# Kernel optimization log

Measured on AMD Instinct MI355X. Metric: run time of the kernel, lower is better.

Reference implementation:

```python
import jax, jax.numpy as jnp
import numpy as np

B, T, C, H = 128, 256, 384, 6
D = C // H  # head dim = 64


def setup_inputs() -> dict:
    key = jax.random.key(0)
    k1, k2, k3, k4, k5 = jax.random.split(key, 5)
    s = 0.02
    return {
        "x": jax.random.normal(k1, (B, T, C), dtype=jnp.float32),
        "W_qkv": jax.random.normal(k2, (C, 3 * C), dtype=jnp.float32) * s,
        "b_qkv": jax.random.normal(k3, (3 * C,), dtype=jnp.float32) * s,
        "W_proj": jax.random.normal(k4, (C, C), dtype=jnp.float32) * s,
        "b_proj": jax.random.normal(k5, (C,), dtype=jnp.float32) * s,
    }


def reference(x, W_qkv, b_qkv, W_proj, b_proj):
    Bv, Tv, Cv = x.shape
    # fused QKV projection, then split
    qkv = x @ W_qkv + b_qkv                      # [B,T,3C]
    q, k, v = jnp.split(qkv, 3, axis=-1)
    # [B,T,C] -> [B,H,T,D]
    q = q.reshape(Bv, Tv, H, D).transpose(0, 2, 1, 3)
    k = k.reshape(Bv, Tv, H, D).transpose(0, 2, 1, 3)
    v = v.reshape(Bv, Tv, H, D).transpose(0, 2, 1, 3)
    # causal masked scores, scaled by head_dim**-0.5
    scores = jnp.einsum("bhqd,bhkd->bhqk", q, k) * (D ** -0.5)
    causal = jnp.tril(jnp.ones((Tv, Tv), dtype=bool))
    scores = jnp.where(causal, scores, -jnp.inf)
    wt = jax.nn.softmax(scores, axis=-1)
    # dropout layers are identity in eval mode
    out = jnp.einsum("bhqk,bhkd->bhqd", wt, v)   # [B,H,T,D]
    out = out.transpose(0, 2, 1, 3).reshape(Bv, Tv, Cv)
    return out @ W_proj + b_proj
```

## Files before the change

### kernel.cpp

```cpp
#include <hip/hip_runtime.h>

typedef unsigned short u16;
typedef unsigned int u32;
typedef __attribute__((ext_vector_type(4))) float f32x4;
typedef __attribute__((ext_vector_type(8))) __bf16 bf16x8;
typedef __attribute__((ext_vector_type(2))) __bf16 bf16x2;

#define NEGINF (-1e30f)
#define QSCALE 0.18033688011112042f

__device__ __forceinline__ u16 f32_to_bf16(float f) {
  union { float f; unsigned int u; } v;
  v.f = f;
  unsigned int u = v.u;
  u += 0x7fffu + ((u >> 16) & 1u);
  return (u16)(u >> 16);
}

__device__ __forceinline__ u32 pk_bf16(float a, float b) {
  bf16x2 t;
  t.x = (__bf16)a;
  t.y = (__bf16)b;
  return __builtin_bit_cast(u32, t);
}

__device__ __forceinline__ f32x4 mfma_bf16(bf16x8 a, bf16x8 b, f32x4 c) {
  return __builtin_amdgcn_mfma_f32_16x16x32_bf16(a, b, c, 0, 0, 0);
}

#define GLOAD_LDS16(g, l) __builtin_amdgcn_global_load_lds( \
    (const __attribute__((address_space(1))) unsigned int*)(g), \
    (__attribute__((address_space(3))) unsigned int*)(l), 16, 0, 0)

__global__ void k_cvt_all(const float4* __restrict__ x4, u16* __restrict__ xb,
                          const float* __restrict__ Wqkv, u16* __restrict__ wqkvb,
                          const float* __restrict__ Wproj, u16* __restrict__ wprojb) {
  const int bidx = (int)blockIdx.x;
  if (bidx < 12288) {
    int i = bidx * 256 + threadIdx.x;
    float4 v = x4[i];
    uint2 o;
    o.x = (unsigned int)f32_to_bf16(v.x) | ((unsigned int)f32_to_bf16(v.y) << 16);
    o.y = (unsigned int)f32_to_bf16(v.z) | ((unsigned int)f32_to_bf16(v.w) << 16);
    *(uint2*)(xb + (size_t)i * 4) = o;
  } else if (bidx < 14016) {
    int idx = (bidx - 12288) * 256 + threadIdx.x;
    if (idx < 384 * 1152) {
      int k = idx / 1152, n = idx - k * 1152;
      wqkvb[(size_t)n * 384 + k] = f32_to_bf16(Wqkv[idx]);
    }
  } else {
    int idx = (bidx - 14016) * 256 + threadIdx.x;
    if (idx < 384 * 384) {
      int k = idx / 384, n = idx - k * 384;
      wprojb[(size_t)n * 384 + k] = f32_to_bf16(Wproj[idx]);
    }
  }
}

template <bool SW>
__device__ __forceinline__ void gemm256x64(
    const u16* __restrict__ A, const u16* __restrict__ Bt,
    int mBase, int nBase, u16* lsA, u16* lsB,
    f32x4 acc[4][2], int lane, int wv, int wm, int wn) {
  const int l15 = lane & 15;
  size_t aoff[4];
  u32 aldso[4];
#pragma unroll
  for (int jj = 0; jj < 4; ++jj) {
    int c = wv * 256 + jj * 64 + lane;
    int row = c >> 3;
    int kc = (c & 7) ^ (row & 7);
    aoff[jj] = (size_t)(mBase + row) * 384 + kc * 8;
    aldso[jj] = (u32)(wv * 256 + jj * 64) * 8;
  }
  int cb = wv * 64 + lane;
  int brow = cb >> 3;
  size_t boff = (size_t)(nBase + brow) * 384 + (size_t)(((cb & 7) ^ (brow & 7)) * 8);
  u32 bldso = (u32)(wv * 64) * 8;

#define STAGE_T(kt, buf) do { \
  _Pragma("unroll") \
  for (int jj = 0; jj < 4; ++jj) \
    GLOAD_LDS16(A + aoff[jj] + (kt), lsA + (buf) * 16384 + aldso[jj]); \
  GLOAD_LDS16(Bt + boff + (kt), lsB + (buf) * 4096 + bldso); \
  } while (0)

  STAGE_T(0, 0);
#pragma unroll
  for (int t = 0; t < 6; ++t) {
    const int cur = t & 1;
    if (t < 5) {
      STAGE_T((t + 1) * 64, cur ^ 1);
      asm volatile("s_waitcnt vmcnt(5)" ::: "memory");
    } else {
      asm volatile("s_waitcnt vmcnt(0)" ::: "memory");
    }
    __builtin_amdgcn_s_barrier();
    const char* bA = (const char*)(lsA + cur * 16384);
    const char* bB = (const char*)(lsB + cur * 4096);
#pragma unroll
    for (int ks = 0; ks < 2; ++ks) {
      bf16x8 af[4], bfr[2];
#pragma unroll
      for (int i = 0; i < 4; ++i) {
        int row = wm * 64 + i * 16 + l15;
        af[i] = *(const bf16x8*)(bA + row * 128 + (((ks * 4 + (lane >> 4)) ^ (row & 7)) << 4));
      }
#pragma unroll
      for (int j = 0; j < 2; ++j) {
        int row = wn * 32 + j * 16 + l15;
        bfr[j] = *(const bf16x8*)(bB + row * 128 + (((ks * 4 + (lane >> 4)) ^ (row & 7)) << 4));
      }
#pragma unroll
      for (int i = 0; i < 4; ++i)
#pragma unroll
        for (int j = 0; j < 2; ++j)
          acc[i][j] = SW ? mfma_bf16(bfr[j], af[i], acc[i][j])
                         : mfma_bf16(af[i], bfr[j], acc[i][j]);
    }
    __builtin_amdgcn_s_barrier();
  }
#undef STAGE_T
}

__global__ __launch_bounds__(512, 4) void k_qkv(
    const u16* __restrict__ A, const u16* __restrict__ Bt,
    const float* __restrict__ bias,
    u16* __restrict__ Qb, u16* __restrict__ Kb, u16* __restrict__ Vtb) {
  __shared__ __align__(16) u16 lsA[2 * 16384];
  __shared__ __align__(16) u16 lsB[2 * 4096];
  const int tid = threadIdx.x, lane = tid & 63, wv = tid >> 6;
  const int l15 = lane & 15, g = lane >> 4;
  const int wm = wv >> 1, wn = wv & 1;
  const int bid = (int)blockIdx.x;
  const int wgid = (bid & 7) * 288 + (bid >> 3);
  const int mtile = wgid / 18, ntile = wgid % 18;
  const int mBase = mtile * 256, nBase = ntile * 64;
  const int part = ntile / 6;
  const int hh = ntile % 6;
  char* ot = (char*)lsA;

  f32x4 acc[4][2] = {};
  if (part == 2) {
    gemm256x64<false>(A, Bt, mBase, nBase, lsA, lsB, acc, lane, wv, wm, wn);
#pragma unroll
    for (int j = 0; j < 2; ++j) {
      int drow = wn * 32 + j * 16 + l15;
      float bv = bias[nBase + drow];
#pragma unroll
      for (int i = 0; i < 4; ++i) {
        int t0 = wm * 64 + i * 16 + g * 4;
        uint2 w;
        w.x = pk_bf16(acc[i][j][0] + bv, acc[i][j][1] + bv);
        w.y = pk_bf16(acc[i][j][2] + bv, acc[i][j][3] + bv);
        int byte = (drow * 512 + t0 * 2) ^ ((drow & 7) << 4);
        *(uint2*)(ot + byte) = w;
      }
    }
    asm volatile("s_waitcnt lgkmcnt(0)" ::: "memory");
    __builtin_amdgcn_s_barrier();
    size_t obase = (size_t)(mtile * 6 + hh) * (64 * 256);
#pragma unroll
    for (int p = 0; p < 4; ++p) {
      int idx = p * 512 + tid;
      int row = idx >> 5, c = idx & 31;
      uint4 v = *(const uint4*)(ot + row * 512 + (((c ^ (row & 7)) << 4)));
      *(uint4*)(Vtb + obase + (size_t)row * 256 + c * 8) = v;
    }
  } else {
    gemm256x64<true>(A, Bt, mBase, nBase, lsA, lsB, acc, lane, wv, wm, wn);
    const float scale = (part == 0) ? QSCALE : 1.0f;
    u16* dst = (part == 0) ? Qb : Kb;
#pragma unroll
    for (int j = 0; j < 2; ++j) {
      int dbase = wn * 32 + j * 16 + g * 4;
      float4 bv4 = *(const float4*)(bias + nBase + dbase);
#pragma unroll
      for (int i = 0; i < 4; ++i) {
        int trow = wm * 64 + i * 16 + l15;
        uint2 w;
        w.x = pk_bf16((acc[i][j][0] + bv4.x) * scale, (acc[i][j][1] + bv4.y) * scale);
        w.y = pk_bf16((acc[i][j][2] + bv4.z) * scale, (acc[i][j][3] + bv4.w) * scale);
        int byte = (trow * 128 + dbase * 2) ^ ((trow & 7) << 4);
        *(uint2*)(ot + byte) = w;
      }
    }
    asm volatile("s_waitcnt lgkmcnt(0)" ::: "memory");
    __builtin_amdgcn_s_barrier();
    size_t obase = (size_t)(mtile * 6 + hh) * (256 * 64);
#pragma unroll
    for (int p = 0; p < 4; ++p) {
      int idx = p * 512 + tid;
      int row = idx >> 3, c = idx & 7;
      uint4 v = *(const uint4*)(ot + row * 128 + (((c ^ (row & 7)) << 4)));
      *(uint4*)(dst + obase + (size_t)row * 64 + c * 8) = v;
    }
  }
}

__global__ __launch_bounds__(256, 3) void k_attn(
    const u16* __restrict__ Qb, const u16* __restrict__ Kb,
    const u16* __restrict__ Vtb, u16* __restrict__ Ob) {
  __shared__ __align__(16) u16 lsP[4][32 * 64];
  const int lane = threadIdx.x & 63, wv = threadIdx.x >> 6;
  const int l15 = lane & 15, g = lane >> 4;
  const int s = blockIdx.y ? (5 - wv) : ((wv < 2) ? 7 - wv : 3 - wv);
  const int bh = blockIdx.x;
  const int b = bh / 6, h = bh % 6;
  const u16* Qh = Qb + (size_t)bh * (256 * 64);
  const u16* Kh = Kb + (size_t)bh * (256 * 64);
  const u16* Vh = Vtb + (size_t)bh * (64 * 256);
  const int ktiles = (s >> 1) + 1;
  char* pbuf = (char*)&lsP[wv][0];

  bf16x8 qf[2][2];
#pragma unroll
  for (int ks = 0; ks < 2; ++ks)
#pragma unroll
    for (int iq = 0; iq < 2; ++iq)
      qf[ks][iq] = *(const bf16x8*)(Qh + (size_t)(s * 32 + iq * 16 + l15) * 64 + ks * 32 + g * 8);

  f32x4 o[4][2] = {};
  float rl[2] = {0.f, 0.f};

#pragma unroll 1
  for (int kt = 0; kt < ktiles; ++kt) {
    bf16x8 kf[2][4];
#pragma unroll
    for (int ks = 0; ks < 2; ++ks)
#pragma unroll
      for (int jk = 0; jk < 4; ++jk)
        kf[ks][jk] = *(const bf16x8*)(Kh + (size_t)(kt * 64 + jk * 16 + l15) * 64 + ks * 32 + g * 8);

    f32x4 st[4][2] = {};
    __builtin_amdgcn_s_setprio(1);
#pragma unroll
    for (int ks = 0; ks < 2; ++ks)
#pragma unroll
      for (int jk = 0; jk < 4; ++jk)
#pragma unroll
        for (int iq = 0; iq < 2; ++iq)
          st[jk][iq] = mfma_bf16(kf[ks][jk], qf[ks][iq], st[jk][iq]);
    __builtin_amdgcn_s_setprio(0);

    bf16x8 vf[2][4];
#pragma unroll
    for (int ks = 0; ks < 2; ++ks)
#pragma unroll
      for (int jd = 0; jd < 4; ++jd)
        vf[ks][jd] = *(const bf16x8*)(Vh + (size_t)(jd * 16 + l15) * 256 + kt * 64 + ks * 32 + g * 8);

    if (kt == ktiles - 1) {
#pragma unroll
      for (int jk = 0; jk < 4; ++jk)
#pragma unroll
        for (int iq = 0; iq < 2; ++iq)
#pragma unroll
          for (int r = 0; r < 4; ++r)
            if (kt * 64 + jk * 16 + g * 4 + r > s * 32 + iq * 16 + l15)
              st[jk][iq][r] = NEGINF;
    }

    float rs[2] = {0.f, 0.f};
#pragma unroll
    for (int jk = 0; jk < 4; ++jk)
#pragma unroll
      for (int iq = 0; iq < 2; ++iq) {
        float p0 = __builtin_amdgcn_exp2f(st[jk][iq][0]);
        float p1 = __builtin_amdgcn_exp2f(st[jk][iq][1]);
        float p2 = __builtin_amdgcn_exp2f(st[jk][iq][2]);
        float p3 = __builtin_amdgcn_exp2f(st[jk][iq][3]);
        rs[iq] += (p0 + p1) + (p2 + p3);
        int q = iq * 16 + l15;
        int byte = (q * 128 + (jk * 16 + g * 4) * 2) ^ ((q & 7) << 4);
        uint2 w;
        w.x = pk_bf16(p0, p1);
        w.y = pk_bf16(p2, p3);
        *(uint2*)(pbuf + byte) = w;
      }
#pragma unroll
    for (int iq = 0; iq < 2; ++iq) {
      float v = rs[iq];
      v += __shfl_xor(v, 16);
      v += __shfl_xor(v, 32);
      rl[iq] += v;
    }

#pragma unroll
    for (int ks = 0; ks < 2; ++ks) {
      bf16x8 pf[2];
#pragma unroll
      for (int iq = 0; iq < 2; ++iq) {
        int q = iq * 16 + l15;
        pf[iq] = *(const bf16x8*)(pbuf + ((q * 128 + ks * 64 + g * 16) ^ ((q & 7) << 4)));
      }
      __builtin_amdgcn_s_setprio(1);
#pragma unroll
      for (int jd = 0; jd < 4; ++jd)
#pragma unroll
        for (int iq = 0; iq < 2; ++iq)
          o[jd][iq] = mfma_bf16(vf[ks][jd], pf[iq], o[jd][iq]);
      __builtin_amdgcn_s_setprio(0);
    }
  }

#pragma unroll
  for (int iq = 0; iq < 2; ++iq) {
    float inv = 1.0f / rl[iq];
    int q = iq * 16 + l15;
#pragma unroll
    for (int jd = 0; jd < 4; ++jd) {
      uint2 w;
      w.x = pk_bf16(o[jd][iq][0] * inv, o[jd][iq][1] * inv);
      w.y = pk_bf16(o[jd][iq][2] * inv, o[jd][iq][3] * inv);
      int byte = (q * 128 + jd * 32 + g * 8) ^ ((q & 7) << 4);
      *(uint2*)(pbuf + byte) = w;
    }
  }
  asm volatile("s_waitcnt lgkmcnt(0)" ::: "memory");
#pragma unroll
  for (int rep = 0; rep < 4; ++rep) {
    int row = rep * 8 + (lane >> 3);
    int c = lane & 7;
    uint4 v = *(const uint4*)(pbuf + row * 128 + ((c ^ (row & 7)) * 16));
    int t = s * 32 + row;
    *(uint4*)(Ob + ((size_t)(b * 256 + t)) * 384 + h * 64 + c * 8) = v;
  }
}

__device__ __forceinline__ void gemm128sq(
    const u16* __restrict__ A, const u16* __restrict__ Bt,
    int mBase, int nBase, u16* lsA, u16* lsB,
    f32x4 acc[4][4], int lane, int wv) {
  const int l15 = lane & 15, g = lane >> 4;
  const int wm = wv >> 1, wn = wv & 1;
  size_t aoff[4], boff[4];
  u32 ldso[4];
#pragma unroll
  for (int jj = 0; jj < 4; ++jj) {
    int c = jj * 256 + wv * 64 + lane;
    int row = c >> 3;
    int kc = (c & 7) ^ (row & 7);
    aoff[jj] = (size_t)(mBase + row) * 384 + kc * 8;
    boff[jj] = (size_t)(nBase + row) * 384 + kc * 8;
    ldso[jj] = (u32)c * 8;
  }
#pragma unroll 1
  for (int t = 0; t < 6; ++t) {
#pragma unroll
    for (int jj = 0; jj < 4; ++jj) {
      GLOAD_LDS16(A + aoff[jj] + t * 64, lsA + ldso[jj]);
      GLOAD_LDS16(Bt + boff[jj] + t * 64, lsB + ldso[jj]);
    }
    __syncthreads();
#pragma unroll
    for (int ks = 0; ks < 2; ++ks) {
      bf16x8 af[4], bfr[4];
#pragma unroll
      for (int i = 0; i < 4; ++i) {
        int row = wm * 64 + i * 16 + l15;
        af[i] = *(const bf16x8*)((const char*)lsA + row * 128 + (((ks * 4 + g) ^ (row & 7)) << 4));
      }
#pragma unroll
      for (int j = 0; j < 4; ++j) {
        int row = wn * 64 + j * 16 + l15;
        bfr[j] = *(const bf16x8*)((const char*)lsB + row * 128 + (((ks * 4 + g) ^ (row & 7)) << 4));
      }
      __builtin_amdgcn_s_setprio(1);
#pragma unroll
      for (int i = 0; i < 4; ++i)
#pragma unroll
        for (int j = 0; j < 4; ++j)
          acc[i][j] = mfma_bf16(af[i], bfr[j], acc[i][j]);
      __builtin_amdgcn_s_setprio(0);
    }
    __syncthreads();
  }
}

__global__ __launch_bounds__(256, 3) void k_proj(
    const u16* __restrict__ A, const u16* __restrict__ Bt,
    const float* __restrict__ bias, float* __restrict__ out) {
  __shared__ __align__(16) u16 lsA[8192];
  __shared__ __align__(16) u16 lsB[8192];
  const int tid = threadIdx.x, lane = tid & 63, wv = tid >> 6;
  const int l15 = lane & 15, g = lane >> 4;
  const int wm = wv >> 1, wn = wv & 1;
  const int bid = (int)blockIdx.x;
  const int wgid = (bid & 7) * 96 + (bid >> 3);
  const int mBase = (wgid / 3) * 128, nBase = (wgid % 3) * 128;
  f32x4 acc[4][4] = {};
  gemm128sq(A, Bt, mBase, nBase, lsA, lsB, acc, lane, wv);
#pragma unroll
  for (int j = 0; j < 4; ++j) {
    int col = nBase + wn * 64 + j * 16 + l15;
    float bv = bias[col];
#pragma unroll
    for (int i = 0; i < 4; ++i) {
      int m0 = mBase + wm * 64 + i * 16 + g * 4;
#pragma unroll
      for (int r = 0; r < 4; ++r)
        out[(size_t)(m0 + r) * 384 + col] = acc[i][j][r] + bv;
    }
  }
}

extern "C" void kernel_launch(void* const* d_in, const int* in_sizes, int n_in,
                              void* d_out, int out_size, void* d_ws, size_t ws_size,
                              hipStream_t stream) {
  const float* x     = (const float*)d_in[0];
  const float* Wqkv  = (const float*)d_in[1];
  const float* bqkv  = (const float*)d_in[2];
  const float* Wproj = (const float*)d_in[3];
  const float* bproj = (const float*)d_in[4];
  float* out = (float*)d_out;

  char* ws = (char*)d_ws;
  u16* xb     = (u16*)(ws);
  u16* wqkvb  = (u16*)(ws + 25165824);
  u16* wprojb = (u16*)(ws + 26050560);
  u16* Qb     = (u16*)(ws + 26345472);
  u16* Kb     = (u16*)(ws + 51511296);
  u16* Vtb    = (u16*)(ws + 76677120);
  u16* Ob     = (u16*)(ws + 101842944);

  k_cvt_all<<<14592, 256, 0, stream>>>((const float4*)x, xb, Wqkv, wqkvb, Wproj, wprojb);
  k_qkv<<<2304, 512, 0, stream>>>(xb, wqkvb, bqkv, Qb, Kb, Vtb);
  k_attn<<<dim3(768, 2), 256, 0, stream>>>(Qb, Kb, Vtb, Ob);
  k_proj<<<768, 256, 0, stream>>>(Ob, wprojb, bproj, out);
}
```

Baseline: 117.1 us.

## Retile QKV GEMM to 128x64 with triple-buffered LDS pipeline

The QKV projection kernel moves from 256x64 tiles with 512 threads and double buffering to 128x64 tiles with 256 threads and a three-stage LDS ring. The prefetch now runs two stages ahead and the trailing barrier is gone. MFMA blocks are wrapped in s_setprio so math waves get priority. Twice as many workgroups give finer load balance. The cost is more total B-tile loads and changed occupancy bounds, and removing the second barrier relies on the three-buffer rotation to avoid overwriting a stage still being read.

```diff
diff --git a/kernel.cpp b/kernel.cpp
--- a/kernel.cpp
+++ b/kernel.cpp
@@ -59,46 +59,54 @@
 }
 
 template <bool SW>
-__device__ __forceinline__ void gemm256x64(
+__device__ __forceinline__ void gemm128x64_p3(
     const u16* __restrict__ A, const u16* __restrict__ Bt,
     int mBase, int nBase, u16* lsA, u16* lsB,
     f32x4 acc[4][2], int lane, int wv, int wm, int wn) {
+  const int tid = wv * 64 + lane;
   const int l15 = lane & 15;
-  size_t aoff[4];
-  u32 aldso[4];
+  size_t aoff[4]; u32 aldso[4];
 #pragma unroll
   for (int jj = 0; jj < 4; ++jj) {
-    int c = wv * 256 + jj * 64 + lane;
+    int c = jj * 256 + tid;
     int row = c >> 3;
     int kc = (c & 7) ^ (row & 7);
     aoff[jj] = (size_t)(mBase + row) * 384 + kc * 8;
-    aldso[jj] = (u32)(wv * 256 + jj * 64) * 8;
-  }
-  int cb = wv * 64 + lane;
-  int brow = cb >> 3;
-  size_t boff = (size_t)(nBase + brow) * 384 + (size_t)(((cb & 7) ^ (brow & 7)) * 8);
-  u32 bldso = (u32)(wv * 64) * 8;
-
-#define STAGE_T(kt, buf) do { \
+    aldso[jj] = (u32)c * 8;
+  }
+  size_t boff[2]; u32 bldso[2];
+#pragma unroll
+  for (int jj = 0; jj < 2; ++jj) {
+    int c = jj * 256 + tid;
+    int row = c >> 3;
+    int kc = (c & 7) ^ (row & 7);
+    boff[jj] = (size_t)(nBase + row) * 384 + kc * 8;
+    bldso[jj] = (u32)c * 8;
+  }
+
+#define STAGE3(kt, buf) do { \
   _Pragma("unroll") \
   for (int jj = 0; jj < 4; ++jj) \
-    GLOAD_LDS16(A + aoff[jj] + (kt), lsA + (buf) * 16384 + aldso[jj]); \
-  GLOAD_LDS16(Bt + boff + (kt), lsB + (buf) * 4096 + bldso); \
+    GLOAD_LDS16(A + aoff[jj] + (kt), lsA + (buf) * 8192 + aldso[jj]); \
+  _Pragma("unroll") \
+  for (int jj = 0; jj < 2; ++jj) \
+    GLOAD_LDS16(Bt + boff[jj] + (kt), lsB + (buf) * 4096 + bldso[jj]); \
   } while (0)
 
-  STAGE_T(0, 0);
+  STAGE3(0, 0);
+  STAGE3(64, 1);
 #pragma unroll
   for (int t = 0; t < 6; ++t) {
-    const int cur = t & 1;
     if (t < 5) {
-      STAGE_T((t + 1) * 64, cur ^ 1);
-      asm volatile("s_waitcnt vmcnt(5)" ::: "memory");
+      asm volatile("s_waitcnt vmcnt(6)" ::: "memory");
     } else {
       asm volatile("s_waitcnt vmcnt(0)" ::: "memory");
     }
     __builtin_amdgcn_s_barrier();
-    const char* bA = (const char*)(lsA + cur * 16384);
-    const char* bB = (const char*)(lsB + cur * 4096);
+    __builtin_amdgcn_sched_barrier(0);
+    if (t < 4) STAGE3((t + 2) * 64, (t + 2) % 3);
+    const char* bA = (const char*)(lsA + (t % 3) * 8192);
+    const char* bB = (const char*)(lsB + (t % 3) * 4096);
 #pragma unroll
     for (int ks = 0; ks < 2; ++ks) {
       bf16x8 af[4], bfr[2];
@@ -112,64 +120,66 @@
         int row = wn * 32 + j * 16 + l15;
         bfr[j] = *(const bf16x8*)(bB + row * 128 + (((ks * 4 + (lane >> 4)) ^ (row & 7)) << 4));
       }
+      __builtin_amdgcn_s_setprio(1);
 #pragma unroll
       for (int i = 0; i < 4; ++i)
 #pragma unroll
         for (int j = 0; j < 2; ++j)
           acc[i][j] = SW ? mfma_bf16(bfr[j], af[i], acc[i][j])
                          : mfma_bf16(af[i], bfr[j], acc[i][j]);
-    }
-    __builtin_amdgcn_s_barrier();
-  }
-#undef STAGE_T
-}
-
-__global__ __launch_bounds__(512, 4) void k_qkv(
+      __builtin_amdgcn_s_setprio(0);
+    }
+  }
+#undef STAGE3
+}
+
+__global__ __launch_bounds__(256, 2) void k_qkv(
     const u16* __restrict__ A, const u16* __restrict__ Bt,
     const float* __restrict__ bias,
     u16* __restrict__ Qb, u16* __restrict__ Kb, u16* __restrict__ Vtb) {
-  __shared__ __align__(16) u16 lsA[2 * 16384];
-  __shared__ __align__(16) u16 lsB[2 * 4096];
+  __shared__ __align__(16) u16 lsA[3 * 8192];
+  __shared__ __align__(16) u16 lsB[3 * 4096];
   const int tid = threadIdx.x, lane = tid & 63, wv = tid >> 6;
   const int l15 = lane & 15, g = lane >> 4;
   const int wm = wv >> 1, wn = wv & 1;
   const int bid = (int)blockIdx.x;
-  const int wgid = (bid & 7) * 288 + (bid >> 3);
+  const int wgid = (bid & 7) * 576 + (bid >> 3);
   const int mtile = wgid / 18, ntile = wgid % 18;
-  const int mBase = mtile * 256, nBase = ntile * 64;
+  const int mBase = mtile * 128, nBase = ntile * 64;
   const int part = ntile / 6;
   const int hh = ntile % 6;
+  const size_t bhh = (size_t)((mtile >> 1) * 6 + hh);
+  const int tt0 = (mtile & 1) * 128;
   char* ot = (char*)lsA;
 
   f32x4 acc[4][2] = {};
   if (part == 2) {
-    gemm256x64<false>(A, Bt, mBase, nBase, lsA, lsB, acc, lane, wv, wm, wn);
+    gemm128x64_p3<false>(A, Bt, mBase, nBase, lsA, lsB, acc, lane, wv, wm, wn);
 #pragma unroll
     for (int j = 0; j < 2; ++j) {
       int drow = wn * 32 + j * 16 + l15;
       float bv = bias[nBase + drow];
 #pragma unroll
       for (int i = 0; i < 4; ++i) {
-        int t0 = wm * 64 + i * 16 + g * 4;
+        int tl = wm * 64 + i * 16 + g * 4;
         uint2 w;
         w.x = pk_bf16(acc[i][j][0] + bv, acc[i][j][1] + bv);
         w.y = pk_bf16(acc[i][j][2] + bv, acc[i][j][3] + bv);
-        int byte = (drow * 512 + t0 * 2) ^ ((drow & 7) << 4);
+        int byte = (drow * 256 + tl * 2) ^ ((drow & 7) << 4);
         *(uint2*)(ot + byte) = w;
       }
     }
     asm volatile("s_waitcnt lgkmcnt(0)" ::: "memory");
     __builtin_amdgcn_s_barrier();
-    size_t obase = (size_t)(mtile * 6 + hh) * (64 * 256);
 #pragma unroll
     for (int p = 0; p < 4; ++p) {
-      int idx = p * 512 + tid;
-      int row = idx >> 5, c = idx & 31;
-      uint4 v = *(const uint4*)(ot + row * 512 + (((c ^ (row & 7)) << 4)));
-      *(uint4*)(Vtb + obase + (size_t)row * 256 + c * 8) = v;
+      int idx = p * 256 + tid;
+      int row = idx >> 4, c = idx & 15;
+      uint4 v = *(const uint4*)(ot + row * 256 + (((c ^ (row & 7)) << 4)));
+      *(uint4*)(Vtb + (bhh * 64 + row) * 256 + tt0 + c * 8) = v;
     }
   } else {
-    gemm256x64<true>(A, Bt, mBase, nBase, lsA, lsB, acc, lane, wv, wm, wn);
+    gemm128x64_p3<true>(A, Bt, mBase, nBase, lsA, lsB, acc, lane, wv, wm, wn);
     const float scale = (part == 0) ? QSCALE : 1.0f;
     u16* dst = (part == 0) ? Qb : Kb;
 #pragma unroll
@@ -188,13 +198,12 @@
     }
     asm volatile("s_waitcnt lgkmcnt(0)" ::: "memory");
     __builtin_amdgcn_s_barrier();
-    size_t obase = (size_t)(mtile * 6 + hh) * (256 * 64);
 #pragma unroll
     for (int p = 0; p < 4; ++p) {
-      int idx = p * 512 + tid;
+      int idx = p * 256 + tid;
       int row = idx >> 3, c = idx & 7;
       uint4 v = *(const uint4*)(ot + row * 128 + (((c ^ (row & 7)) << 4)));
-      *(uint4*)(dst + obase + (size_t)row * 64 + c * 8) = v;
+      *(uint4*)(dst + (bhh * 256 + tt0 + row) * 64 + c * 8) = v;
     }
   }
 }
@@ -426,7 +435,7 @@
   u16* Ob     = (u16*)(ws + 101842944);
 
   k_cvt_all<<<14592, 256, 0, stream>>>((const float4*)x, xb, Wqkv, wqkvb, Wproj, wprojb);
-  k_qkv<<<2304, 512, 0, stream>>>(xb, wqkvb, bqkv, Qb, Kb, Vtb);
+  k_qkv<<<4608, 256, 0, stream>>>(xb, wqkvb, bqkv, Qb, Kb, Vtb);
   k_attn<<<dim3(768, 2), 256, 0, stream>>>(Qb, Kb, Vtb, Ob);
   k_proj<<<768, 256, 0, stream>>>(Ob, wprojb, bproj, out);
 }
```

Measured after the change: 126.6 us. 1.08x slower.
